# Kernel tuning notes

Hardware: AMD Instinct MI355X
Metric: run time of the kernel (lower is better)

The kernel has to match this reference:

```python
import jax, jax.numpy as jnp
import numpy as np

HEADS = 16
DIM_HEAD = 64
SCALE = 8.0
LN_EPS = 1e-5
L2_EPS = 1e-12


def setup_inputs() -> dict:
    key = jax.random.key(0)
    ks = jax.random.split(key, 4)
    b, n, dim = 4, 2048, 1024
    inner = HEADS * DIM_HEAD
    return {
        "x": jax.random.normal(ks[0], (b, n, dim), dtype=jnp.float32),
        "gamma": jnp.ones((dim,), jnp.float32),
        "beta": jnp.zeros((dim,), jnp.float32),
        "null_kv": jax.random.normal(ks[1], (2, HEADS, 1, DIM_HEAD), dtype=jnp.float32),
        "Wq": jax.random.normal(ks[2], (dim, inner), dtype=jnp.float32) * 0.02,
        "Wkv": jax.random.normal(ks[3], (dim, 2 * inner), dtype=jnp.float32) * 0.02,
        "q_scale": jnp.ones((DIM_HEAD,), jnp.float32),
        "k_scale": jnp.ones((DIM_HEAD,), jnp.float32),
        "Wo": jax.random.normal(jax.random.fold_in(key, 7), (inner, dim), dtype=jnp.float32) * 0.02,
    }


def _l2norm(t):
    # matches F.normalize(dim=-1, eps=1e-12): divide by max(||t||, eps)
    nrm = jnp.sqrt(jnp.sum(t * t, axis=-1, keepdims=True))
    return t / jnp.maximum(nrm, L2_EPS)


def reference(x, gamma, beta, null_kv, Wq, Wkv, q_scale, k_scale, Wo):
    b, n, dim = x.shape
    # LayerNorm with learned gamma, zero beta buffer
    mu = jnp.mean(x, axis=-1, keepdims=True)
    var = jnp.mean((x - mu) ** 2, axis=-1, keepdims=True)
    xn = (x - mu) / jnp.sqrt(var + LN_EPS) * gamma + beta

    q = xn @ Wq                       # [b, n, inner]
    kv = xn @ Wkv                     # [b, n, 2*inner]
    k, v = jnp.split(kv, 2, axis=-1)

    def to_heads(t):
        return t.reshape(b, n, HEADS, DIM_HEAD).transpose(0, 2, 1, 3)  # b h n d

    q, k, v = map(to_heads, (q, k, v))

    nk = jnp.broadcast_to(null_kv[0], (b, HEADS, 1, DIM_HEAD))
    nv = jnp.broadcast_to(null_kv[1], (b, HEADS, 1, DIM_HEAD))
    k = jnp.concatenate([nk, k], axis=2)  # [b, h, n+1, d]
    v = jnp.concatenate([nv, v], axis=2)

    q = _l2norm(q) * q_scale
    k = _l2norm(k) * k_scale

    sim = jnp.einsum("bhid,bhjd->bhij", q, k) * SCALE
    attn = jax.nn.softmax(sim, axis=-1)
    out = jnp.einsum("bhij,bhjd->bhid", attn, v)  # [b, h, n, d]
    out = out.transpose(0, 2, 1, 3).reshape(b, n, HEADS * DIM_HEAD)
    return out @ Wo
```

## Files before the change

### kernel.cpp

```cpp
#include <hip/hip_runtime.h>

typedef unsigned short u16;
typedef unsigned int u32;
typedef short bf16x8 __attribute__((ext_vector_type(8)));
typedef unsigned short u16x8 __attribute__((ext_vector_type(8)));
typedef float f32x4 __attribute__((ext_vector_type(4)));

#define HEADS 16
#define DHEAD 64
#define NTOK 2048
#define DIM 1024
#define MROWS 8192
#define NKPAD 2176
#define NKVALID 2049
#define GLDS 72
#define SP 72
#define BQ 256

__device__ __forceinline__ float bf2f(u16 h) {
  return __uint_as_float(((unsigned)h) << 16);
}
__device__ __forceinline__ u16 f2bf(float f) {
  unsigned u = __float_as_uint(f);
  u += 0x7FFF + ((u >> 16) & 1);
  return (u16)(u >> 16);
}
__device__ __forceinline__ f32x4 mfma16(bf16x8 a, bf16x8 b, f32x4 c) {
  return __builtin_amdgcn_mfma_f32_16x16x32_bf16(a, b, c, 0, 0, 0);
}
__device__ __forceinline__ f32x4 zero4() {
  f32x4 z; z[0] = 0.f; z[1] = 0.f; z[2] = 0.f; z[3] = 0.f; return z;
}
__device__ __forceinline__ float load1(const void* p, int i, int isbf) {
  return isbf ? bf2f(((const u16*)p)[i]) : ((const float*)p)[i];
}
__device__ __forceinline__ u32 pack_bf2(float a, float b) {
  return __builtin_amdgcn_perm(__float_as_uint(b) + 0x8000u,
                               __float_as_uint(a) + 0x8000u, 0x07060302u);
}
__device__ __forceinline__ void gl16(const u16* g, u16* l) {
  __builtin_amdgcn_global_load_lds(
      (const __attribute__((address_space(1))) u32*)g,
      (__attribute__((address_space(3))) u32*)l, 16, 0, 0);
}
__device__ __forceinline__ int swa(int r, int cc) {
  return ((r >> 3) << 9) + ((r & 7) << 6) + ((cc ^ (r & 7)) << 3);
}

__global__ __launch_bounds__(64) void detect_kernel(const u16* __restrict__ gamma,
                                                    int* __restrict__ flag)
{
  if (threadIdx.x == 0) *flag = (gamma[0] == (u16)0x3F80) ? 1 : 0;
}

__global__ __launch_bounds__(256) void ln_kernel(const void* __restrict__ x,
    const void* __restrict__ gamma, const void* __restrict__ beta,
    const int* __restrict__ flagp, u16* __restrict__ xn)
{
  int isbf = *flagp;
  int row = blockIdx.x, t = threadIdx.x;
  float v0, v1, v2, v3;
  if (isbf) {
    ushort4 raw = ((const ushort4*)x)[row * 256 + t];
    v0 = bf2f(raw.x); v1 = bf2f(raw.y); v2 = bf2f(raw.z); v3 = bf2f(raw.w);
  } else {
    float4 raw = ((const float4*)x)[row * 256 + t];
    v0 = raw.x; v1 = raw.y; v2 = raw.z; v3 = raw.w;
  }
  float s = v0 + v1 + v2 + v3;
  float q = v0 * v0 + v1 * v1 + v2 * v2 + v3 * v3;
#pragma unroll
  for (int off = 32; off; off >>= 1) {
    s += __shfl_xor(s, off, 64);
    q += __shfl_xor(q, off, 64);
  }
  __shared__ float red[4][2];
  int wv = t >> 6, lane = t & 63;
  if (lane == 0) { red[wv][0] = s; red[wv][1] = q; }
  __syncthreads();
  float ts = red[0][0] + red[1][0] + red[2][0] + red[3][0];
  float tq = red[0][1] + red[1][1] + red[2][1] + red[3][1];
  float mu = ts * (1.0f / DIM);
  float var = tq * (1.0f / DIM) - mu * mu;
  float rs = rsqrtf(var + 1e-5f);
  ushort4 o;
  o.x = f2bf((v0 - mu) * rs * load1(gamma, t * 4 + 0, isbf) + load1(beta, t * 4 + 0, isbf));
  o.y = f2bf((v1 - mu) * rs * load1(gamma, t * 4 + 1, isbf) + load1(beta, t * 4 + 1, isbf));
  o.z = f2bf((v2 - mu) * rs * load1(gamma, t * 4 + 2, isbf) + load1(beta, t * 4 + 2, isbf));
  o.w = f2bf((v3 - mu) * rs * load1(gamma, t * 4 + 3, isbf) + load1(beta, t * 4 + 3, isbf));
  ((ushort4*)(xn + (size_t)row * DIM))[t] = o;
}

__global__ __launch_bounds__(256) void transpose_any(const void* __restrict__ src,
    u16* __restrict__ dst, int R, int C, const int* __restrict__ flagp)
{
  int isbf = *flagp;
  __shared__ __align__(16) u16 tile[64][65];
  int tc = blockIdx.x * 64, tr = blockIdx.y * 64;
  int t = threadIdx.x;
  int cr = t >> 4, cc = (t & 15) * 4;
#pragma unroll
  for (int rr = 0; rr < 64; rr += 16) {
    size_t e = (size_t)(tr + cr + rr) * C + tc + cc;
    u16 a, b, c, d;
    if (isbf) {
      ushort4 v = *(const ushort4*)((const u16*)src + e);
      a = v.x; b = v.y; c = v.z; d = v.w;
    } else {
      float4 v = *(const float4*)((const float*)src + e);
      a = f2bf(v.x); b = f2bf(v.y); c = f2bf(v.z); d = f2bf(v.w);
    }
    tile[cr + rr][cc + 0] = a; tile[cr + rr][cc + 1] = b;
    tile[cr + rr][cc + 2] = c; tile[cr + rr][cc + 3] = d;
  }
  __syncthreads();
#pragma unroll
  for (int rr = 0; rr < 64; rr += 16) {
    int dr = cr + rr;
    ushort4 w;
    w.x = tile[cc + 0][dr]; w.y = tile[cc + 1][dr];
    w.z = tile[cc + 2][dr]; w.w = tile[cc + 3][dr];
    *(ushort4*)&dst[(size_t)(tc + dr) * R + tr + cc] = w;
  }
}

__global__ __launch_bounds__(256) void fill_null(const void* __restrict__ nullkv,
    const void* __restrict__ k_scale, const int* __restrict__ flagp,
    u16* __restrict__ kb, u16* __restrict__ vt)
{
  int isbf = *flagp;
  int bh = blockIdx.x, h = bh & 15, t = threadIdx.x;
  if (t < 64) {
    float nk = load1(nullkv, h * 64 + t, isbf);
    float nv = load1(nullkv, 1024 + h * 64 + t, isbf);
    float ss = nk * nk;
#pragma unroll
    for (int off = 32; off; off >>= 1) ss += __shfl_xor(ss, off, 64);
    float rn = 1.0f / fmaxf(sqrtf(ss), 1e-12f);
    kb[((size_t)bh * NKPAD + 2048) * DHEAD + t] =
        f2bf(nk * rn * load1(k_scale, t, isbf));
    vt[((size_t)bh * DHEAD + t) * NKPAD + 2048] = f2bf(nv);
  }
  for (int idx = t; idx < 127 * 64; idx += 256) {
    kb[((size_t)bh * NKPAD + 2049) * DHEAD + idx] = 0;
  }
  {
    int d = t & 63, rep = t >> 6;
    u16* row = vt + ((size_t)bh * DHEAD + d) * NKPAD;
#pragma unroll
    for (int k = 0; k < 32; k++) {
      int j = 2049 + rep * 32 + k;
      if (j < NKPAD) row[j] = 0;
    }
  }
}

__device__ __forceinline__ void gemm_mainloop(const u16* __restrict__ Arow,
    const u16* __restrict__ Btrow, int K, u16* sA, u16* sB, f32x4 acc[4][4])
{
  int t = threadIdx.x;
  int lane = t & 63, wv = t >> 6;
  int wx = wv & 1, wy = wv >> 1;
  int l15 = lane & 15, quad = lane >> 4;
#pragma unroll
  for (int mt = 0; mt < 4; mt++)
#pragma unroll
    for (int nt = 0; nt < 4; nt++) acc[mt][nt] = zero4();
  int r8 = lane >> 3, xx = lane & 7;
  int cc0 = xx ^ r8;
  for (int k0 = 0; k0 < K; k0 += 64) {
#pragma unroll
    for (int c = 0; c < 4; c++) {
      int chunk = wv * 4 + c;
      size_t go = (size_t)(chunk * 8 + r8) * K + k0 + cc0 * 8;
      gl16(&Arow[go], &sA[chunk * 512]);
      gl16(&Btrow[go], &sB[chunk * 512]);
    }
    __syncthreads();
#pragma unroll
    for (int ks = 0; ks < 2; ks++) {
      bf16x8 af[4], bfr[4];
#pragma unroll
      for (int mt = 0; mt < 4; mt++)
        af[mt] = *(const bf16x8*)&sA[swa(wy * 64 + mt * 16 + l15, ks * 4 + quad)];
#pragma unroll
      for (int nt = 0; nt < 4; nt++)
        bfr[nt] = *(const bf16x8*)&sB[swa(wx * 64 + nt * 16 + l15, ks * 4 + quad)];
#pragma unroll
      for (int mt = 0; mt < 4; mt++)
#pragma unroll
        for (int nt = 0; nt < 4; nt++)
          acc[mt][nt] = mfma16(af[mt], bfr[nt], acc[mt][nt]);
    }
    __syncthreads();
  }
}

__global__ __launch_bounds__(256) void gemm_qkv(const u16* __restrict__ xn,
    const u16* __restrict__ wqT, const u16* __restrict__ wkvT,
    const void* __restrict__ q_scale, const void* __restrict__ k_scale,
    const int* __restrict__ flagp,
    u16* __restrict__ qb, u16* __restrict__ kb, u16* __restrict__ vt)
{
  int isbf = *flagp;
  __shared__ __align__(16) u16 sA[16 * 512];
  __shared__ __align__(16) u16 sB[16 * 512];
  int n0 = blockIdx.x * 128, m0 = blockIdx.y * 128;
  const u16* Bt = (n0 < DIM) ? (wqT + (size_t)n0 * DIM)
                             : (wkvT + (size_t)(n0 - DIM) * DIM);
  f32x4 acc[4][4];
  gemm_mainloop(xn + (size_t)m0 * DIM, Bt, DIM, sA, sB, acc);

  int t = threadIdx.x, lane = t & 63, wv = t >> 6;
  int wx = wv & 1, wy = wv >> 1, l15 = lane & 15, quad = lane >> 4;
  int region = n0 >> 10;
  int rc = (n0 & 1023) + wx * 64;
  int h = rc >> 6;
  int bq = m0 >> 11;

  if (region == 2) {
    int i0 = (m0 & 2047) + wy * 64 + quad * 4;
#pragma unroll
    for (int mt = 0; mt < 4; mt++) {
#pragma unroll
      for (int nt = 0; nt < 4; nt++) {
        int d = nt * 16 + l15;
        ushort4 w;
        w.x = f2bf(acc[mt][nt][0]); w.y = f2bf(acc[mt][nt][1]);
        w.z = f2bf(acc[mt][nt][2]); w.w = f2bf(acc[mt][nt][3]);
        *(ushort4*)&vt[((size_t)((bq * HEADS + h) * DHEAD + d)) * NKPAD
                       + i0 + mt * 16] = w;
      }
    }
    return;
  }

  float sc[4];
#pragma unroll
  for (int nt = 0; nt < 4; nt++)
    sc[nt] = (region == 0) ? load1(q_scale, nt * 16 + l15, isbf) * 8.0f
                           : load1(k_scale, nt * 16 + l15, isbf);
#pragma unroll
  for (int mt = 0; mt < 4; mt++) {
#pragma unroll
    for (int r = 0; r < 4; r++) {
      int R = m0 + wy * 64 + mt * 16 + quad * 4 + r;
      int i = R & 2047;
      int bh = bq * HEADS + h;
      float v0 = acc[mt][0][r], v1 = acc[mt][1][r];
      float v2 = acc[mt][2][r], v3 = acc[mt][3][r];
      float ss = v0 * v0 + v1 * v1 + v2 * v2 + v3 * v3;
#pragma unroll
      for (int off = 8; off; off >>= 1) ss += __shfl_xor(ss, off, 64);
      float rn = 1.0f / fmaxf(sqrtf(ss), 1e-12f);
      v0 *= rn * sc[0]; v1 *= rn * sc[1]; v2 *= rn * sc[2]; v3 *= rn * sc[3];
      u16* dst = (region == 0) ? qb + ((size_t)bh * NTOK + i) * DHEAD
                               : kb + ((size_t)bh * NKPAD + i) * DHEAD;
      dst[0 * 16 + l15] = f2bf(v0);
      dst[1 * 16 + l15] = f2bf(v1);
      dst[2 * 16 + l15] = f2bf(v2);
      dst[3 * 16 + l15] = f2bf(v3);
    }
  }
}

__global__ __launch_bounds__(256, 2) void attn_kernel(const u16* __restrict__ qg,
    const u16* __restrict__ kg, const u16* __restrict__ vtg,
    const void* __restrict__ q_scale, const void* __restrict__ k_scale,
    const int* __restrict__ flagp, u16* __restrict__ og)
{
  int isbf = *flagp;
  __shared__ __align__(16) u16 sK[64][GLDS];
  __shared__ __align__(16) u16 sVT[64][GLDS];
  __shared__ __align__(16) u16 sP[4][64][SP];
  int bh = blockIdx.y, q0 = blockIdx.x * BQ;
  int b = bh >> 4, hh = bh & 15;
  int t = threadIdx.x, lane = t & 63, wv = t >> 6;
  int l15 = lane & 15, quad = lane >> 4;

  float pm = fabsf(load1(q_scale, lane, isbf) * load1(k_scale, lane, isbf));
#pragma unroll
  for (int off = 32; off; off >>= 1) pm = fmaxf(pm, __shfl_xor(pm, off, 64));
  float Mb = pm * 8.0f;

  bf16x8 bq[4][2];
  const u16* qbase = qg + ((size_t)bh * NTOK + q0 + wv * 64) * DHEAD;
#pragma unroll
  for (int it = 0; it < 4; it++)
#pragma unroll
    for (int ks = 0; ks < 2; ks++)
      bq[it][ks] = *(const bf16x8*)&qbase[(it * 16 + l15) * DHEAD + ks * 32 + quad * 8];

  f32x4 Oa[4][4];
  float lsum[4];
#pragma unroll
  for (int it = 0; it < 4; it++) {
#pragma unroll
    for (int dt = 0; dt < 4; dt++) Oa[it][dt] = zero4();
    lsum[it] = 0.f;
  }

  int srow = t >> 3, scol = (t & 7) * 8;
  const u16* kgb = kg + (size_t)bh * NKPAD * DHEAD;
  const u16* vgb = vtg + (size_t)bh * DHEAD * NKPAD;

  u16x8 kpre[2], vpre[2];
#pragma unroll
  for (int p = 0; p < 2; p++) {
    int r = srow + p * 32;
    kpre[p] = *(const u16x8*)&kgb[(size_t)r * DHEAD + scol];
    vpre[p] = *(const u16x8*)&vgb[(size_t)r * NKPAD + scol];
  }

  for (int j0 = 0; j0 < 2112; j0 += 64) {
    __syncthreads();
#pragma unroll
    for (int p = 0; p < 2; p++) {
      int r = srow + p * 32;
      *(u16x8*)&sK[r][scol] = kpre[p];
      *(u16x8*)&sVT[r][scol] = vpre[p];
    }
    int jn = j0 + 64;
    if (jn < 2112) {
#pragma unroll
      for (int p = 0; p < 2; p++) {
        int r = srow + p * 32;
        kpre[p] = *(const u16x8*)&kgb[(size_t)(jn + r) * DHEAD + scol];
        vpre[p] = *(const u16x8*)&vgb[(size_t)r * NKPAD + jn + scol];
      }
    }
    __syncthreads();

    bf16x8 ak[4][2];
#pragma unroll
    for (int ks = 0; ks < 2; ks++)
#pragma unroll
      for (int jt = 0; jt < 4; jt++)
        ak[jt][ks] = *(const bf16x8*)&sK[jt * 16 + l15][ks * 32 + quad * 8];

    bool tail = (j0 >= 2048);
#pragma unroll
    for (int jt = 0; jt < 4; jt++) {
      f32x4 st[4];
#pragma unroll
      for (int it = 0; it < 4; it++) st[it] = zero4();
#pragma unroll
      for (int ks = 0; ks < 2; ks++)
#pragma unroll
        for (int it = 0; it < 4; it++)
          st[it] = mfma16(ak[jt][ks], bq[it][ks], st[it]);
      if (!tail) {
#pragma unroll
        for (int it = 0; it < 4; it++) {
          float p0 = __expf(st[it][0] - Mb), p1 = __expf(st[it][1] - Mb);
          float p2 = __expf(st[it][2] - Mb), p3 = __expf(st[it][3] - Mb);
          lsum[it] += (p0 + p1) + (p2 + p3);
          uint2 w; w.x = pack_bf2(p0, p1); w.y = pack_bf2(p2, p3);
          *(uint2*)&sP[wv][it * 16 + l15][jt * 16 + quad * 4] = w;
        }
      } else {
        int jb = j0 + jt * 16 + quad * 4;
#pragma unroll
        for (int it = 0; it < 4; it++) {
          float p0 = (jb + 0 < NKVALID) ? __expf(st[it][0] - Mb) : 0.f;
          float p1 = (jb + 1 < NKVALID) ? __expf(st[it][1] - Mb) : 0.f;
          float p2 = (jb + 2 < NKVALID) ? __expf(st[it][2] - Mb) : 0.f;
          float p3 = (jb + 3 < NKVALID) ? __expf(st[it][3] - Mb) : 0.f;
          lsum[it] += (p0 + p1) + (p2 + p3);
          uint2 w; w.x = pack_bf2(p0, p1); w.y = pack_bf2(p2, p3);
          *(uint2*)&sP[wv][it * 16 + l15][jt * 16 + quad * 4] = w;
        }
      }
    }

    bf16x8 bv[4][2];
#pragma unroll
    for (int jk = 0; jk < 2; jk++)
#pragma unroll
      for (int dt = 0; dt < 4; dt++)
        bv[dt][jk] = *(const bf16x8*)&sVT[dt * 16 + l15][jk * 32 + quad * 8];
#pragma unroll
    for (int it = 0; it < 4; it++)
#pragma unroll
      for (int jk = 0; jk < 2; jk++) {
        bf16x8 ap = *(const bf16x8*)&sP[wv][it * 16 + l15][jk * 32 + quad * 8];
#pragma unroll
        for (int dt = 0; dt < 4; dt++)
          Oa[it][dt] = mfma16(ap, bv[dt][jk], Oa[it][dt]);
      }
  }

#pragma unroll
  for (int it = 0; it < 4; it++) {
    lsum[it] += __shfl_xor(lsum[it], 16, 64);
    lsum[it] += __shfl_xor(lsum[it], 32, 64);
  }
#pragma unroll
  for (int it = 0; it < 4; it++) {
#pragma unroll
    for (int r = 0; r < 4; r++) {
      int sl = (lane & 48) + ((lane >> 4) << 2) + r;
      float linv = 1.0f / __shfl(lsum[it], sl, 64);
      int i = q0 + wv * 64 + it * 16 + quad * 4 + r;
      u16* dst = og + ((size_t)(b * NTOK + i)) * DIM + hh * DHEAD;
      dst[0 * 16 + l15] = f2bf(Oa[it][0][r] * linv);
      dst[1 * 16 + l15] = f2bf(Oa[it][1][r] * linv);
      dst[2 * 16 + l15] = f2bf(Oa[it][2][r] * linv);
      dst[3 * 16 + l15] = f2bf(Oa[it][3][r] * linv);
    }
  }
}

__global__ __launch_bounds__(256) void gemm_out(const u16* __restrict__ og,
    const u16* __restrict__ woT, const int* __restrict__ flagp,
    void* __restrict__ outp)
{
  int isbf = *flagp;
  __shared__ __align__(16) u16 sA[16 * 512];
  __shared__ __align__(16) u16 sB[16 * 512];
  int n0 = blockIdx.x * 128, m0 = blockIdx.y * 128;
  f32x4 acc[4][4];
  gemm_mainloop(og + (size_t)m0 * DIM, woT + (size_t)n0 * DIM, DIM, sA, sB, acc);
  int t = threadIdx.x, lane = t & 63, wv = t >> 6;
  int wx = wv & 1, wy = wv >> 1, l15 = lane & 15, quad = lane >> 4;
#pragma unroll
  for (int mt = 0; mt < 4; mt++) {
#pragma unroll
    for (int r = 0; r < 4; r++) {
      int R = m0 + wy * 64 + mt * 16 + quad * 4 + r;
      size_t base = (size_t)R * DIM + n0 + wx * 64;
      if (isbf) {
        u16* dst = (u16*)outp + base;
        dst[0 * 16 + l15] = f2bf(acc[mt][0][r]);
        dst[1 * 16 + l15] = f2bf(acc[mt][1][r]);
        dst[2 * 16 + l15] = f2bf(acc[mt][2][r]);
        dst[3 * 16 + l15] = f2bf(acc[mt][3][r]);
      } else {
        float* dst = (float*)outp + base;
        dst[0 * 16 + l15] = acc[mt][0][r];
        dst[1 * 16 + l15] = acc[mt][1][r];
        dst[2 * 16 + l15] = acc[mt][2][r];
        dst[3 * 16 + l15] = acc[mt][3][r];
      }
    }
  }
}

extern "C" void kernel_launch(void* const* d_in, const int* in_sizes, int n_in,
                              void* d_out, int out_size, void* d_ws, size_t ws_size,
                              hipStream_t stream) {
  const void* x       = d_in[0];
  const void* gamma   = d_in[1];
  const void* beta    = d_in[2];
  const void* null_kv = d_in[3];
  const void* Wq      = d_in[4];
  const void* Wkv     = d_in[5];
  const void* q_scale = d_in[6];
  const void* k_scale = d_in[7];
  const void* Wo      = d_in[8];

  char* ws = (char*)d_ws;
  size_t off = 256;
  int* flag = (int*)ws;
  auto alloc = [&](size_t elems) {
    u16* p = (u16*)(ws + off);
    off += ((elems * 2 + 255) & ~(size_t)255);
    return p;
  };
  u16* xn   = alloc((size_t)MROWS * DIM);
  u16* wqT  = alloc((size_t)1024 * 1024);
  u16* wkvT = alloc((size_t)2048 * 1024);
  u16* woT  = alloc((size_t)1024 * 1024);
  u16* qb   = alloc((size_t)64 * NTOK * DHEAD);
  u16* kb   = alloc((size_t)64 * NKPAD * DHEAD);
  u16* vt   = alloc((size_t)64 * DHEAD * NKPAD);
  u16* og   = xn;

  detect_kernel<<<1, 64, 0, stream>>>((const u16*)gamma, flag);
  ln_kernel<<<MROWS, 256, 0, stream>>>(x, gamma, beta, flag, xn);
  transpose_any<<<dim3(16, 16), 256, 0, stream>>>(Wq, wqT, 1024, 1024, flag);
  transpose_any<<<dim3(32, 16), 256, 0, stream>>>(Wkv, wkvT, 1024, 2048, flag);
  transpose_any<<<dim3(16, 16), 256, 0, stream>>>(Wo, woT, 1024, 1024, flag);
  gemm_qkv<<<dim3(24, 64), 256, 0, stream>>>(xn, wqT, wkvT, q_scale, k_scale,
                                             flag, qb, kb, vt);
  fill_null<<<64, 256, 0, stream>>>(null_kv, k_scale, flag, kb, vt);
  attn_kernel<<<dim3(NTOK / BQ, 64), 256, 0, stream>>>(qb, kb, vt, q_scale,
                                                       k_scale, flag, og);
  gemm_out<<<dim3(8, 64), 256, 0, stream>>>(og, woT, flag, d_out);
}
```

Baseline: 334.1 us.

## Load K/V MFMA fragments directly from global, drop shared staging and barriers

The attention kernel no longer stages K and V^T tiles through shared memory with two barriers per iteration. Each wave now loads its MFMA operand fragments for K (prefetched one tile ahead) and V^T straight from global memory into registers. The grid is also reordered so blocks sharing a head are adjacent, which should help L2 reuse of K/V across the four waves and eight q-blocks. The trade-off is that every wave issues its own redundant global loads and the V loads are not prefetched, so latency may be exposed, and register pressure rises.

```diff
diff --git a/kernel.cpp b/kernel.cpp
--- a/kernel.cpp
+++ b/kernel.cpp
@@ -13,7 +13,6 @@
 #define MROWS 8192
 #define NKPAD 2176
 #define NKVALID 2049
-#define GLDS 72
 #define SP 72
 #define BQ 256
 
@@ -270,10 +269,8 @@
     const int* __restrict__ flagp, u16* __restrict__ og)
 {
   int isbf = *flagp;
-  __shared__ __align__(16) u16 sK[64][GLDS];
-  __shared__ __align__(16) u16 sVT[64][GLDS];
   __shared__ __align__(16) u16 sP[4][64][SP];
-  int bh = blockIdx.y, q0 = blockIdx.x * BQ;
+  int bh = blockIdx.x, q0 = blockIdx.y * BQ;
   int b = bh >> 4, hh = bh & 15;
   int t = threadIdx.x, lane = t & 63, wv = t >> 6;
   int l15 = lane & 15, quad = lane >> 4;
@@ -300,43 +297,33 @@
     lsum[it] = 0.f;
   }
 
-  int srow = t >> 3, scol = (t & 7) * 8;
   const u16* kgb = kg + (size_t)bh * NKPAD * DHEAD;
   const u16* vgb = vtg + (size_t)bh * DHEAD * NKPAD;
 
-  u16x8 kpre[2], vpre[2];
-#pragma unroll
-  for (int p = 0; p < 2; p++) {
-    int r = srow + p * 32;
-    kpre[p] = *(const u16x8*)&kgb[(size_t)r * DHEAD + scol];
-    vpre[p] = *(const u16x8*)&vgb[(size_t)r * NKPAD + scol];
-  }
+  bf16x8 kf[8], kn[8], vf[8];
+#pragma unroll
+  for (int jt = 0; jt < 4; jt++)
+#pragma unroll
+    for (int ks = 0; ks < 2; ks++)
+      kf[jt * 2 + ks] = *(const bf16x8*)&kgb[(size_t)(jt * 16 + l15) * DHEAD
+                                             + ks * 32 + quad * 8];
 
   for (int j0 = 0; j0 < 2112; j0 += 64) {
-    __syncthreads();
-#pragma unroll
-    for (int p = 0; p < 2; p++) {
-      int r = srow + p * 32;
-      *(u16x8*)&sK[r][scol] = kpre[p];
-      *(u16x8*)&sVT[r][scol] = vpre[p];
-    }
+#pragma unroll
+    for (int dt = 0; dt < 4; dt++)
+#pragma unroll
+      for (int jk = 0; jk < 2; jk++)
+        vf[dt * 2 + jk] = *(const bf16x8*)&vgb[(size_t)(dt * 16 + l15) * NKPAD
+                                               + j0 + jk * 32 + quad * 8];
     int jn = j0 + 64;
     if (jn < 2112) {
 #pragma unroll
-      for (int p = 0; p < 2; p++) {
-        int r = srow + p * 32;
-        kpre[p] = *(const u16x8*)&kgb[(size_t)(jn + r) * DHEAD + scol];
-        vpre[p] = *(const u16x8*)&vgb[(size_t)r * NKPAD + jn + scol];
-      }
-    }
-    __syncthreads();
-
-    bf16x8 ak[4][2];
-#pragma unroll
-    for (int ks = 0; ks < 2; ks++)
-#pragma unroll
       for (int jt = 0; jt < 4; jt++)
-        ak[jt][ks] = *(const bf16x8*)&sK[jt * 16 + l15][ks * 32 + quad * 8];
+#pragma unroll
+        for (int ks = 0; ks < 2; ks++)
+          kn[jt * 2 + ks] = *(const bf16x8*)&kgb[(size_t)(jn + jt * 16 + l15) * DHEAD
+                                                 + ks * 32 + quad * 8];
+    }
 
     bool tail = (j0 >= 2048);
 #pragma unroll
@@ -348,7 +335,7 @@
       for (int ks = 0; ks < 2; ks++)
 #pragma unroll
         for (int it = 0; it < 4; it++)
-          st[it] = mfma16(ak[jt][ks], bq[it][ks], st[it]);
+          st[it] = mfma16(kf[jt * 2 + ks], bq[it][ks], st[it]);
       if (!tail) {
 #pragma unroll
         for (int it = 0; it < 4; it++) {
@@ -373,12 +360,6 @@
       }
     }
 
-    bf16x8 bv[4][2];
-#pragma unroll
-    for (int jk = 0; jk < 2; jk++)
-#pragma unroll
-      for (int dt = 0; dt < 4; dt++)
-        bv[dt][jk] = *(const bf16x8*)&sVT[dt * 16 + l15][jk * 32 + quad * 8];
 #pragma unroll
     for (int it = 0; it < 4; it++)
 #pragma unroll
@@ -386,8 +367,10 @@
         bf16x8 ap = *(const bf16x8*)&sP[wv][it * 16 + l15][jk * 32 + quad * 8];
 #pragma unroll
         for (int dt = 0; dt < 4; dt++)
-          Oa[it][dt] = mfma16(ap, bv[dt][jk], Oa[it][dt]);
+          Oa[it][dt] = mfma16(ap, vf[dt * 2 + jk], Oa[it][dt]);
       }
+#pragma unroll
+    for (int i = 0; i < 8; i++) kf[i] = kn[i];
   }
 
 #pragma unroll
@@ -484,7 +467,7 @@
   gemm_qkv<<<dim3(24, 64), 256, 0, stream>>>(xn, wqT, wkvT, q_scale, k_scale,
                                              flag, qb, kb, vt);
   fill_null<<<64, 256, 0, stream>>>(null_kv, k_scale, flag, kb, vt);
-  attn_kernel<<<dim3(NTOK / BQ, 64), 256, 0, stream>>>(qb, kb, vt, q_scale,
+  attn_kernel<<<dim3(64, NTOK / BQ), 256, 0, stream>>>(qb, kb, vt, q_scale,
                                                        k_scale, flag, og);
   gemm_out<<<dim3(8, 64), 256, 0, stream>>>(og, woT, flag, d_out);
 }
```

Result: slower. 357.4 us (+6.9%).

## Halve attention P buffer, raise occupancy, and stage V-transpose stores via LDS

Applied to the files above, without the earlier changes.

The attention kernel now computes P in two 32-key halves, so the per-wave P tile in shared memory shrinks from 72 to 40 columns and the launch bound asks for 4 blocks per CU instead of 2. The grid axes are swapped so consecutive blocks share the same head, which may improve cache reuse of K and V. In the QKV GEMM epilogue, the V output is transposed through LDS and written with 16-byte coalesced stores instead of scattered 8-byte ones. Forcing 4 blocks per CU may cap registers and cause spills, and there is a sync hazard: the V-transpose reuses the mainloop's shared memory without an extra barrier.

```diff
diff --git a/kernel.cpp b/kernel.cpp
--- a/kernel.cpp
+++ b/kernel.cpp
@@ -14,7 +14,7 @@
 #define NKPAD 2176
 #define NKVALID 2049
 #define GLDS 72
-#define SP 72
+#define SP 40
 #define BQ 256
 
 __device__ __forceinline__ float bf2f(u16 h) {
@@ -203,8 +203,9 @@
     u16* __restrict__ qb, u16* __restrict__ kb, u16* __restrict__ vt)
 {
   int isbf = *flagp;
-  __shared__ __align__(16) u16 sA[16 * 512];
-  __shared__ __align__(16) u16 sB[16 * 512];
+  __shared__ __align__(16) u16 smem[18432];
+  u16* sA = smem;
+  u16* sB = smem + 8192;
   int n0 = blockIdx.x * 128, m0 = blockIdx.y * 128;
   const u16* Bt = (n0 < DIM) ? (wqT + (size_t)n0 * DIM)
                              : (wkvT + (size_t)(n0 - DIM) * DIM);
@@ -219,18 +220,25 @@
   int bq = m0 >> 11;
 
   if (region == 2) {
-    int i0 = (m0 & 2047) + wy * 64 + quad * 4;
+    u16* sT = smem + wv * (64 * 72);
 #pragma unroll
     for (int mt = 0; mt < 4; mt++) {
 #pragma unroll
       for (int nt = 0; nt < 4; nt++) {
-        int d = nt * 16 + l15;
-        ushort4 w;
-        w.x = f2bf(acc[mt][nt][0]); w.y = f2bf(acc[mt][nt][1]);
-        w.z = f2bf(acc[mt][nt][2]); w.w = f2bf(acc[mt][nt][3]);
-        *(ushort4*)&vt[((size_t)((bq * HEADS + h) * DHEAD + d)) * NKPAD
-                       + i0 + mt * 16] = w;
+        uint2 w;
+        w.x = pack_bf2(acc[mt][nt][0], acc[mt][nt][1]);
+        w.y = pack_bf2(acc[mt][nt][2], acc[mt][nt][3]);
+        *(uint2*)&sT[(nt * 16 + l15) * 72 + mt * 16 + quad * 4] = w;
       }
+    }
+    int dp = lane >> 3, ip = (lane & 7) * 8;
+    size_t ibase = (size_t)(m0 & 2047) + wy * 64 + ip;
+    u16* vbase = vt + ((size_t)(bq * HEADS + h) * DHEAD) * NKPAD;
+#pragma unroll
+    for (int rep = 0; rep < 8; rep++) {
+      int d = rep * 8 + dp;
+      u16x8 v = *(const u16x8*)&sT[d * 72 + ip];
+      *(u16x8*)&vbase[(size_t)d * NKPAD + ibase] = v;
     }
     return;
   }
@@ -264,7 +272,7 @@
   }
 }
 
-__global__ __launch_bounds__(256, 2) void attn_kernel(const u16* __restrict__ qg,
+__global__ __launch_bounds__(256, 4) void attn_kernel(const u16* __restrict__ qg,
     const u16* __restrict__ kg, const u16* __restrict__ vtg,
     const void* __restrict__ q_scale, const void* __restrict__ k_scale,
     const int* __restrict__ flagp, u16* __restrict__ og)
@@ -273,7 +281,7 @@
   __shared__ __align__(16) u16 sK[64][GLDS];
   __shared__ __align__(16) u16 sVT[64][GLDS];
   __shared__ __align__(16) u16 sP[4][64][SP];
-  int bh = blockIdx.y, q0 = blockIdx.x * BQ;
+  int bh = blockIdx.x, q0 = blockIdx.y * BQ;
   int b = bh >> 4, hh = bh & 15;
   int t = threadIdx.x, lane = t & 63, wv = t >> 6;
   int l15 = lane & 15, quad = lane >> 4;
@@ -283,13 +291,13 @@
   for (int off = 32; off; off >>= 1) pm = fmaxf(pm, __shfl_xor(pm, off, 64));
   float Mb = pm * 8.0f;
 
-  bf16x8 bq[4][2];
+  bf16x8 bqf[4][2];
   const u16* qbase = qg + ((size_t)bh * NTOK + q0 + wv * 64) * DHEAD;
 #pragma unroll
   for (int it = 0; it < 4; it++)
 #pragma unroll
     for (int ks = 0; ks < 2; ks++)
-      bq[it][ks] = *(const bf16x8*)&qbase[(it * 16 + l15) * DHEAD + ks * 32 + quad * 8];
+      bqf[it][ks] = *(const bf16x8*)&qbase[(it * 16 + l15) * DHEAD + ks * 32 + quad * 8];
 
   f32x4 Oa[4][4];
   float lsum[4];
@@ -340,54 +348,53 @@
 
     bool tail = (j0 >= 2048);
 #pragma unroll
-    for (int jt = 0; jt < 4; jt++) {
-      f32x4 st[4];
-#pragma unroll
-      for (int it = 0; it < 4; it++) st[it] = zero4();
-#pragma unroll
-      for (int ks = 0; ks < 2; ks++)
-#pragma unroll
-        for (int it = 0; it < 4; it++)
-          st[it] = mfma16(ak[jt][ks], bq[it][ks], st[it]);
-      if (!tail) {
-#pragma unroll
-        for (int it = 0; it < 4; it++) {
-          float p0 = __expf(st[it][0] - Mb), p1 = __expf(st[it][1] - Mb);
-          float p2 = __expf(st[it][2] - Mb), p3 = __expf(st[it][3] - Mb);
-          lsum[it] += (p0 + p1) + (p2 + p3);
-          uint2 w; w.x = pack_bf2(p0, p1); w.y = pack_bf2(p2, p3);
-          *(uint2*)&sP[wv][it * 16 + l15][jt * 16 + quad * 4] = w;
-        }
-      } else {
-        int jb = j0 + jt * 16 + quad * 4;
-#pragma unroll
-        for (int it = 0; it < 4; it++) {
-          float p0 = (jb + 0 < NKVALID) ? __expf(st[it][0] - Mb) : 0.f;
-          float p1 = (jb + 1 < NKVALID) ? __expf(st[it][1] - Mb) : 0.f;
-          float p2 = (jb + 2 < NKVALID) ? __expf(st[it][2] - Mb) : 0.f;
-          float p3 = (jb + 3 < NKVALID) ? __expf(st[it][3] - Mb) : 0.f;
-          lsum[it] += (p0 + p1) + (p2 + p3);
-          uint2 w; w.x = pack_bf2(p0, p1); w.y = pack_bf2(p2, p3);
-          *(uint2*)&sP[wv][it * 16 + l15][jt * 16 + quad * 4] = w;
+    for (int hf = 0; hf < 2; hf++) {
+#pragma unroll
+      for (int jt2 = 0; jt2 < 2; jt2++) {
+        int jt = hf * 2 + jt2;
+        f32x4 st[4];
+#pragma unroll
+        for (int it = 0; it < 4; it++) st[it] = zero4();
+#pragma unroll
+        for (int ks = 0; ks < 2; ks++)
+#pragma unroll
+          for (int it = 0; it < 4; it++)
+            st[it] = mfma16(ak[jt][ks], bqf[it][ks], st[it]);
+        if (!tail) {
+#pragma unroll
+          for (int it = 0; it < 4; it++) {
+            float p0 = __expf(st[it][0] - Mb), p1 = __expf(st[it][1] - Mb);
+            float p2 = __expf(st[it][2] - Mb), p3 = __expf(st[it][3] - Mb);
+            lsum[it] += (p0 + p1) + (p2 + p3);
+            uint2 w; w.x = pack_bf2(p0, p1); w.y = pack_bf2(p2, p3);
+            *(uint2*)&sP[wv][it * 16 + l15][jt2 * 16 + quad * 4] = w;
+          }
+        } else {
+          int jb = j0 + jt * 16 + quad * 4;
+#pragma unroll
+          for (int it = 0; it < 4; it++) {
+            float p0 = (jb + 0 < NKVALID) ? __expf(st[it][0] - Mb) : 0.f;
+            float p1 = (jb + 1 < NKVALID) ? __expf(st[it][1] - Mb) : 0.f;
+            float p2 = (jb + 2 < NKVALID) ? __expf(st[it][2] - Mb) : 0.f;
+            float p3 = (jb + 3 < NKVALID) ? __expf(st[it][3] - Mb) : 0.f;
+            lsum[it] += (p0 + p1) + (p2 + p3);
+            uint2 w; w.x = pack_bf2(p0, p1); w.y = pack_bf2(p2, p3);
+            *(uint2*)&sP[wv][it * 16 + l15][jt2 * 16 + quad * 4] = w;
+          }
         }
       }
-    }
-
-    bf16x8 bv[4][2];
-#pragma unroll
-    for (int jk = 0; jk < 2; jk++)
+      bf16x8 bv[4];
 #pragma unroll
       for (int dt = 0; dt < 4; dt++)
-        bv[dt][jk] = *(const bf16x8*)&sVT[dt * 16 + l15][jk * 32 + quad * 8];
-#pragma unroll
-    for (int it = 0; it < 4; it++)
-#pragma unroll
-      for (int jk = 0; jk < 2; jk++) {
-        bf16x8 ap = *(const bf16x8*)&sP[wv][it * 16 + l15][jk * 32 + quad * 8];
+        bv[dt] = *(const bf16x8*)&sVT[dt * 16 + l15][hf * 32 + quad * 8];
+#pragma unroll
+      for (int it = 0; it < 4; it++) {
+        bf16x8 ap = *(const bf16x8*)&sP[wv][it * 16 + l15][quad * 8];
 #pragma unroll
         for (int dt = 0; dt < 4; dt++)
-          Oa[it][dt] = mfma16(ap, bv[dt][jk], Oa[it][dt]);
+          Oa[it][dt] = mfma16(ap, bv[dt], Oa[it][dt]);
       }
+    }
   }
 
 #pragma unroll
@@ -484,7 +491,7 @@
   gemm_qkv<<<dim3(24, 64), 256, 0, stream>>>(xn, wqT, wkvT, q_scale, k_scale,
                                              flag, qb, kb, vt);
   fill_null<<<64, 256, 0, stream>>>(null_kv, k_scale, flag, kb, vt);
-  attn_kernel<<<dim3(NTOK / BQ, 64), 256, 0, stream>>>(qb, kb, vt, q_scale,
+  attn_kernel<<<dim3(64, NTOK / BQ), 256, 0, stream>>>(qb, kb, vt, q_scale,
                                                        k_scale, flag, og);
   gemm_out<<<dim3(8, 64), 256, 0, stream>>>(og, woT, flag, d_out);
 }
```

Result: slower. 623.6 us (+86.6%).
